# Kernel optimization log

Hardware: AMD Instinct MI355X
Metric: run time of the kernel (lower is better)

## Reference

```python
import jax, jax.numpy as jnp
import numpy as np

NUM_HEADS = 12
EPS = 1e-4


def setup_inputs() -> dict:
    key = jax.random.key(0)
    k1, k2, k3 = jax.random.split(key, 3)
    C = 768
    B, N = 128, 196  # B = b * num_frames = 8 * 16
    x = jax.random.normal(k1, (B, N, C), dtype=jnp.float32)
    W_qkv = jax.random.normal(k2, (3 * C, C), dtype=jnp.float32) * 0.02
    W_proj = jax.random.normal(k3, (C, C), dtype=jnp.float32) * 0.02
    b_proj = jnp.zeros((C,), dtype=jnp.float32)
    return {"x": x, "W_qkv": W_qkv, "W_proj": W_proj, "b_proj": b_proj,
            "num_frames": 16}


def reference(x, W_qkv, W_proj, b_proj, num_frames):
    B, N, C = x.shape
    h = NUM_HEADS
    e = C // h
    # qkv projection (no bias), split k-first then heads: 'b n (k h e)'
    qkv = (x @ W_qkv.T).reshape(B, N, 3, h, e)
    q, k, v = qkv[:, :, 0], qkv[:, :, 1], qkv[:, :, 2]  # [B, N, h, e]
    q_ = jax.nn.relu(q)
    k_ = jax.nn.relu(k)
    # fold frames into the sequence: (b f) n -> b (f n)
    b = B // num_frames
    S = num_frames * N
    q_ = q_.reshape(b, S, h, e)
    k_ = k_.reshape(b, S, h, e)
    v_ = v.reshape(b, S, h, e)
    # kv trick: kv[b,h,e,d] = sum_s k[b,s,h,e] v[b,s,h,d]
    kv = jnp.einsum('bshe,bshd->bhed', k_, v_)
    k_sum = k_.sum(axis=1)  # [b, h, e]
    z = 1.0 / (jnp.einsum('bshe,bhe->bsh', q_, k_sum) + EPS)  # [b, S, h]
    out = jnp.einsum('bshe,bhed->bshd', q_, kv) * z[..., None]  # [b, S, h, e]
    out = out.reshape(B, N, C)
    # output projection (dropouts are identity at eval)
    return out @ W_proj.T + b_proj
```

## Files before the change

### kernel.cpp

```cpp
#include <hip/hip_runtime.h>
#include <hip/hip_bf16.h>

#define EPS_Z 1e-4f

typedef __attribute__((ext_vector_type(8))) short bf16x8;
typedef __attribute__((ext_vector_type(4))) float f32x4;

__device__ __forceinline__ float b2f(short s) {
    union { unsigned u; float f; } cv;
    cv.u = ((unsigned)(unsigned short)s) << 16;
    return cv.f;
}

__device__ __forceinline__ void gld_lds16(const __hip_bfloat16* g, __hip_bfloat16* l) {
    __builtin_amdgcn_global_load_lds(
        (__attribute__((address_space(1))) void*)(g),
        (__attribute__((address_space(3))) void*)(l),
        16, 0, 0);
}

__global__ __launch_bounds__(256)
void cvt_f32_bf16(const float* __restrict__ in, __hip_bfloat16* __restrict__ out, int n4)
{
    int i = blockIdx.x * 256 + threadIdx.x;
    if (i >= n4) return;
    float4 v = ((const float4*)in)[i];
    union { short4 s; __hip_bfloat16 h[4]; } o;
    o.h[0] = __float2bfloat16(v.x);
    o.h[1] = __float2bfloat16(v.y);
    o.h[2] = __float2bfloat16(v.z);
    o.h[3] = __float2bfloat16(v.w);
    ((short4*)out)[i] = o.s;
}

template<int MODE, typename CT>
__global__ __launch_bounds__(256, 2)
void gemm_bt(const __hip_bfloat16* __restrict__ A,
             const __hip_bfloat16* __restrict__ B,
             CT* __restrict__ C,
             const float* __restrict__ bias,
             int K, int N, int gx)
{
    __shared__ __align__(16) __hip_bfloat16 As[128 * 64];
    __shared__ __align__(16) __hip_bfloat16 Bs[128 * 64];
    const int g = blockIdx.x;
    const int gp = (g & 7) * ((int)gridDim.x >> 3) + (g >> 3);
    const int bx = gp % gx;
    const int by = gp / gx;

    const int tid = threadIdx.x;
    const int w = tid >> 6;
    const int l = tid & 63;
    const int wr = (w >> 1) * 64;
    const int wc = (w & 1) * 64;
    const int l15 = l & 15;
    const int lq = l >> 4;
    const int rx = l15 & 7;

    f32x4 acc[4][4] = {};

    const int srow8 = l >> 3;
    const int scol = (((l & 7) ^ (l >> 3)) << 3);

    const __hip_bfloat16* Ab = A + (size_t)by * 128 * K;
    const __hip_bfloat16* Bb = B + (size_t)bx * 128 * K;

    for (int k0 = 0; k0 < K; k0 += 64) {
        __syncthreads();
        #pragma unroll
        for (int i = 0; i < 4; ++i) {
            const int chunk = w * 4 + i;
            const int row = chunk * 8 + srow8;
            gld_lds16(Ab + (size_t)row * K + (k0 + scol), As + chunk * 512);
            gld_lds16(Bb + (size_t)row * K + (k0 + scol), Bs + chunk * 512);
        }
        __syncthreads();
        #pragma unroll
        for (int kk = 0; kk < 64; kk += 32) {
            const int kb = (kk >> 3) + lq;
            const int col = (kb ^ rx) << 3;
            bf16x8 a[4], b[4];
            #pragma unroll
            for (int i = 0; i < 4; ++i)
                a[i] = *(const bf16x8*)(As + (wr + i * 16 + l15) * 64 + col);
            #pragma unroll
            for (int j = 0; j < 4; ++j)
                b[j] = *(const bf16x8*)(Bs + (wc + j * 16 + l15) * 64 + col);
            #pragma unroll
            for (int i = 0; i < 4; ++i)
                #pragma unroll
                for (int j = 0; j < 4; ++j)
                    acc[i][j] = __builtin_amdgcn_mfma_f32_16x16x32_bf16(a[i], b[j], acc[i][j], 0, 0, 0);
        }
    }

    const int crow0 = by * 128 + wr + lq * 4;
    const int ccol0 = bx * 128 + wc + l15;
    #pragma unroll
    for (int i = 0; i < 4; ++i) {
        #pragma unroll
        for (int j = 0; j < 4; ++j) {
            const int gc = ccol0 + j * 16;
            const float badd = (MODE == 2) ? bias[gc] : 0.0f;
            #pragma unroll
            for (int r = 0; r < 4; ++r) {
                const int gr = crow0 + i * 16 + r;
                float v = acc[i][j][r];
                if (MODE == 1 && gc < 1536) v = fmaxf(v, 0.0f);
                if (MODE == 2) v += badd;
                if (MODE == 1)
                    ((__hip_bfloat16*)C)[(size_t)gr * N + gc] = __float2bfloat16(v);
                else
                    ((float*)C)[(size_t)gr * N + gc] = v;
            }
        }
    }
}

__global__ __launch_bounds__(256)
void kv_mfma_kernel(const __hip_bfloat16* __restrict__ qkv,
                    float* __restrict__ kvg, float* __restrict__ ksumg)
{
    const int SPLIT = 14;
    const int bh = blockIdx.x / SPLIT;
    const int ck = blockIdx.x % SPLIT;
    const int b = bh / 12, h = bh % 12;

    __shared__ __align__(16) __hip_bfloat16 kT[64 * 40];
    __shared__ __align__(16) __hip_bfloat16 vT[64 * 40];

    const int tid = threadIdx.x;
    const int w = tid >> 6, l = tid & 63;
    const int l15 = l & 15, lq = l >> 4;

    const int half = tid >> 7;
    const int idx  = tid & 127;
    const int e0 = (idx >> 4) * 8;
    const int sp = idx & 15;

    const size_t rowbase = (size_t)b * 3136 * 2304 + (half ? 1536 : 768) + h * 64 + e0;
    __hip_bfloat16* Tdst = half ? vT : kT;

    f32x4 acc[4] = {};
    f32x4 accks = {};

    bf16x8 ones;
    #pragma unroll
    for (int i = 0; i < 8; ++i) ones[i] = (short)0x3F80;

    const int s_begin = ck * 224;
    for (int s0 = s_begin; s0 < s_begin + 224; s0 += 32) {
        __syncthreads();
        bf16x8 r0 = *(const bf16x8*)(qkv + rowbase + (size_t)(s0 + 2 * sp) * 2304);
        bf16x8 r1 = *(const bf16x8*)(qkv + rowbase + (size_t)(s0 + 2 * sp + 1) * 2304);
        #pragma unroll
        for (int q = 0; q < 8; ++q) {
            unsigned pk = ((unsigned)(unsigned short)r0[q]) |
                          (((unsigned)(unsigned short)r1[q]) << 16);
            *(unsigned*)(Tdst + (e0 + q) * 40 + 2 * sp) = pk;
        }
        __syncthreads();
        bf16x8 a = *(const bf16x8*)(vT + (w * 16 + l15) * 40 + lq * 8);
        bf16x8 bfr[4];
        #pragma unroll
        for (int j = 0; j < 4; ++j)
            bfr[j] = *(const bf16x8*)(kT + (j * 16 + l15) * 40 + lq * 8);
        #pragma unroll
        for (int j = 0; j < 4; ++j)
            acc[j] = __builtin_amdgcn_mfma_f32_16x16x32_bf16(a, bfr[j], acc[j], 0, 0, 0);
        accks = __builtin_amdgcn_mfma_f32_16x16x32_bf16(ones, bfr[w], accks, 0, 0, 0);
    }

    float* kvdst = kvg + ((size_t)bh << 12);
    #pragma unroll
    for (int j = 0; j < 4; ++j) {
        const int col = j * 16 + l15;
        #pragma unroll
        for (int r = 0; r < 4; ++r) {
            const int row = w * 16 + lq * 4 + r;
            atomicAdd(kvdst + row * 64 + col, acc[j][r]);
        }
    }
    if (lq == 0)
        atomicAdd(ksumg + (bh << 6) + w * 16 + l15, accks[0]);
}

__global__ __launch_bounds__(256)
void attn_mfma2(const __hip_bfloat16* __restrict__ qkv,
                const __hip_bfloat16* __restrict__ kvb,
                const float* __restrict__ ksumg,
                __hip_bfloat16* __restrict__ att)
{
    const int bh = blockIdx.x / 49;
    const int mt = blockIdx.x % 49;
    const int b = bh / 12, h = bh % 12;
    const int tid = threadIdx.x;
    const int w = tid >> 6, l = tid & 63;
    const int l15 = l & 15, lq = l >> 4;

    const size_t m0 = (size_t)b * 3136 + (size_t)mt * 64 + w * 16;

    const __hip_bfloat16* qrow = qkv + (m0 + l15) * 2304 + h * 64;
    bf16x8 aq0 = *(const bf16x8*)(qrow + lq * 8);
    bf16x8 aq1 = *(const bf16x8*)(qrow + 32 + lq * 8);

    const float* ks = ksumg + (bh << 6);
    float kse[8], kse1[8];
    *(float4*)(kse)      = *(const float4*)(ks + lq * 8);
    *(float4*)(kse + 4)  = *(const float4*)(ks + lq * 8 + 4);
    *(float4*)(kse1)     = *(const float4*)(ks + 32 + lq * 8);
    *(float4*)(kse1 + 4) = *(const float4*)(ks + 32 + lq * 8 + 4);
    float zp = 0.0f;
    #pragma unroll
    for (int j = 0; j < 8; ++j)
        zp += b2f(aq0[j]) * kse[j] + b2f(aq1[j]) * kse1[j];
    zp += __shfl_xor(zp, 16);
    zp += __shfl_xor(zp, 32);
    const float zr = 1.0f / (zp + EPS_Z);

    const __hip_bfloat16* kvh = kvb + ((size_t)bh << 12);
    f32x4 acc[4] = {};
    #pragma unroll
    for (int j = 0; j < 4; ++j) {
        bf16x8 b0 = *(const bf16x8*)(kvh + (j * 16 + l15) * 64 + lq * 8);
        bf16x8 b1 = *(const bf16x8*)(kvh + (j * 16 + l15) * 64 + 32 + lq * 8);
        acc[j] = __builtin_amdgcn_mfma_f32_16x16x32_bf16(aq0, b0, acc[j], 0, 0, 0);
        acc[j] = __builtin_amdgcn_mfma_f32_16x16x32_bf16(aq1, b1, acc[j], 0, 0, 0);
    }

    float zrow[4];
    #pragma unroll
    for (int r = 0; r < 4; ++r) zrow[r] = __shfl(zr, lq * 4 + r);

    #pragma unroll
    for (int j = 0; j < 4; ++j) {
        const int col = j * 16 + l15;
        #pragma unroll
        for (int r = 0; r < 4; ++r) {
            const int row = lq * 4 + r;
            att[(m0 + row) * 768 + h * 64 + col] = __float2bfloat16(acc[j][r] * zrow[r]);
        }
    }
}

extern "C" void kernel_launch(void* const* d_in, const int* in_sizes, int n_in,
                              void* d_out, int out_size, void* d_ws, size_t ws_size,
                              hipStream_t stream)
{
    const float* x      = (const float*)d_in[0];
    const float* W_qkv  = (const float*)d_in[1];
    const float* W_proj = (const float*)d_in[2];
    const float* b_proj = (const float*)d_in[3];
    float* out = (float*)d_out;

    const int M = 25088, K = 768, N1 = 2304, N2 = 768;

    __hip_bfloat16* qkv = (__hip_bfloat16*)d_ws;
    __hip_bfloat16* xb  = qkv + (size_t)M * N1;
    __hip_bfloat16* wqb = xb + (size_t)M * K;
    __hip_bfloat16* wpb = wqb + (size_t)N1 * K;
    float* kvg  = (float*)(wpb + (size_t)N2 * K);
    float* ksum = kvg + 96 * 4096;
    __hip_bfloat16* kvb = (__hip_bfloat16*)(ksum + 96 * 64);
    __hip_bfloat16* att = xb;

    hipMemsetAsync(kvg, 0, (size_t)(96 * 4096 + 96 * 64) * sizeof(float), stream);

    cvt_f32_bf16<<<(M * K / 4 + 255) / 256, 256, 0, stream>>>(x, xb, M * K / 4);
    cvt_f32_bf16<<<(N1 * K / 4 + 255) / 256, 256, 0, stream>>>(W_qkv, wqb, N1 * K / 4);
    cvt_f32_bf16<<<(N2 * K / 4 + 255) / 256, 256, 0, stream>>>(W_proj, wpb, N2 * K / 4);

    gemm_bt<1, __hip_bfloat16><<<(M / 128) * (N1 / 128), 256, 0, stream>>>(
        xb, wqb, qkv, nullptr, K, N1, N1 / 128);
    kv_mfma_kernel<<<96 * 14, 256, 0, stream>>>(qkv, kvg, ksum);
    cvt_f32_bf16<<<(96 * 4096 / 4 + 255) / 256, 256, 0, stream>>>(kvg, kvb, 96 * 4096 / 4);
    attn_mfma2<<<96 * 49, 256, 0, stream>>>(qkv, kvb, ksum, att);
    gemm_bt<2, float><<<(M / 128) * (N2 / 128), 256, 0, stream>>>(
        att, wpb, out, b_proj, K, N2, N2 / 128);
}
```

Baseline: 347.1 us.

## Replace QKV GEMM with 256x256 double-buffered pipelined MFMA kernel

Adds a new QKV projection GEMM that uses 256x256 tiles, 512 threads, double-buffered LDS filled by direct global-to-LDS loads, XOR-swizzled LDS layout, and interleaved staging with MFMA phases under explicit waitcnt, barriers and setprio. The ReLU on the q and k columns is applied in the epilogue. The aim is to raise MFMA utilization and overlap memory with compute for the largest GEMM. The cost is high LDS use (128KB per block) and heavy register pressure, and with 98*9 blocks the wave quantization across CUs may be uneven.

```diff
diff --git a/kernel.cpp b/kernel.cpp
--- a/kernel.cpp
+++ b/kernel.cpp
@@ -17,6 +17,14 @@
         (__attribute__((address_space(1))) void*)(g),
         (__attribute__((address_space(3))) void*)(l),
         16, 0, 0);
+}
+
+__device__ __forceinline__ void fence_barrier() {
+    asm volatile("" ::: "memory");
+    __builtin_amdgcn_sched_barrier(0);
+    __builtin_amdgcn_s_barrier();
+    __builtin_amdgcn_sched_barrier(0);
+    asm volatile("" ::: "memory");
 }
 
 __global__ __launch_bounds__(256)
@@ -31,6 +39,174 @@
     o.h[2] = __float2bfloat16(v.z);
     o.h[3] = __float2bfloat16(v.w);
     ((short4*)out)[i] = o.s;
+}
+
+__global__ __launch_bounds__(512, 2)
+void gemm256_relu(const __hip_bfloat16* __restrict__ A,
+                  const __hip_bfloat16* __restrict__ B,
+                  __hip_bfloat16* __restrict__ C,
+                  int K, int N, int gx)
+{
+    __shared__ __align__(16) __hip_bfloat16 As[2][256 * 64];
+    __shared__ __align__(16) __hip_bfloat16 Bs[2][256 * 64];
+
+    const int nwg = (int)gridDim.x;
+    const int g = blockIdx.x;
+    const int xcd = g & 7, lin = g >> 3;
+    const int q = nwg >> 3, r = nwg & 7;
+    const int gp = (xcd < r ? xcd * (q + 1) : r * (q + 1) + (xcd - r) * q) + lin;
+    const int bx = gp % gx, by = gp / gx;
+
+    const int tid = threadIdx.x;
+    const int w = tid >> 6, l = tid & 63;
+    const int l15 = l & 15, lq = l >> 4;
+    const int rx = l15 & 7;
+    const int wr = (w >> 2) * 128;
+    const int wc = (w & 3) * 64;
+    const int srow8 = l >> 3;
+    const int scol = ((l & 7) ^ srow8) << 3;
+
+    const __hip_bfloat16* Ab = A + (size_t)by * 256 * K;
+    const __hip_bfloat16* Bb = B + (size_t)bx * 256 * K;
+
+    f32x4 acc[8][4] = {};
+    const int NT = K >> 6;
+
+#define STAGE_A(buf_, half_, t_) do { \
+    const int k0_ = (t_) << 6; \
+    const int c0_ = (half_) * 16 + w * 2; \
+    gld_lds16(Ab + (size_t)(c0_ * 8 + srow8) * K + (k0_ + scol), &As[buf_][c0_ * 512]); \
+    gld_lds16(Ab + (size_t)((c0_ + 1) * 8 + srow8) * K + (k0_ + scol), &As[buf_][(c0_ + 1) * 512]); \
+} while (0)
+#define STAGE_B(buf_, half_, t_) do { \
+    const int k0_ = (t_) << 6; \
+    const int c0_ = (half_) * 16 + w * 2; \
+    gld_lds16(Bb + (size_t)(c0_ * 8 + srow8) * K + (k0_ + scol), &Bs[buf_][c0_ * 512]); \
+    gld_lds16(Bb + (size_t)((c0_ + 1) * 8 + srow8) * K + (k0_ + scol), &Bs[buf_][(c0_ + 1) * 512]); \
+} while (0)
+
+    STAGE_B(0, 0, 0); STAGE_B(0, 1, 0);
+    STAGE_A(0, 0, 0); STAGE_A(0, 1, 0);
+    STAGE_B(1, 0, 1); STAGE_B(1, 1, 1);
+    asm volatile("s_waitcnt vmcnt(4)" ::: "memory");
+    fence_barrier();
+
+    for (int t = 0; t < NT; ++t) {
+        const int buf = t & 1;
+        const __hip_bfloat16* Asb = As[buf];
+        const __hip_bfloat16* Bsb = Bs[buf];
+        bf16x8 bfr[4][2];
+        bf16x8 afr[2][2];
+
+        #pragma unroll
+        for (int j = 0; j < 4; ++j)
+            #pragma unroll
+            for (int ks = 0; ks < 2; ++ks)
+                bfr[j][ks] = *(const bf16x8*)(Bsb + (wc + j * 16 + l15) * 64 + (((ks * 4 + lq) ^ rx) << 3));
+        #pragma unroll
+        for (int d = 0; d < 2; ++d)
+            #pragma unroll
+            for (int ks = 0; ks < 2; ++ks)
+                afr[d][ks] = *(const bf16x8*)(Asb + (wr + (0 + d) * 16 + l15) * 64 + (((ks * 4 + lq) ^ rx) << 3));
+        if (t + 1 < NT) STAGE_A(buf ^ 1, 0, t + 1);
+        fence_barrier();
+        asm volatile("s_waitcnt lgkmcnt(0)" ::: "memory");
+        __builtin_amdgcn_sched_barrier(0);
+        __builtin_amdgcn_s_setprio(1);
+        #pragma unroll
+        for (int d = 0; d < 2; ++d)
+            #pragma unroll
+            for (int j = 0; j < 4; ++j)
+                #pragma unroll
+                for (int ks = 0; ks < 2; ++ks)
+                    acc[0 + d][j] = __builtin_amdgcn_mfma_f32_16x16x32_bf16(afr[d][ks], bfr[j][ks], acc[0 + d][j], 0, 0, 0);
+        __builtin_amdgcn_s_setprio(0);
+        fence_barrier();
+
+        #pragma unroll
+        for (int d = 0; d < 2; ++d)
+            #pragma unroll
+            for (int ks = 0; ks < 2; ++ks)
+                afr[d][ks] = *(const bf16x8*)(Asb + (wr + (2 + d) * 16 + l15) * 64 + (((ks * 4 + lq) ^ rx) << 3));
+        if (t + 1 < NT) STAGE_A(buf ^ 1, 1, t + 1);
+        fence_barrier();
+        asm volatile("s_waitcnt lgkmcnt(0)" ::: "memory");
+        __builtin_amdgcn_sched_barrier(0);
+        __builtin_amdgcn_s_setprio(1);
+        #pragma unroll
+        for (int d = 0; d < 2; ++d)
+            #pragma unroll
+            for (int j = 0; j < 4; ++j)
+                #pragma unroll
+                for (int ks = 0; ks < 2; ++ks)
+                    acc[2 + d][j] = __builtin_amdgcn_mfma_f32_16x16x32_bf16(afr[d][ks], bfr[j][ks], acc[2 + d][j], 0, 0, 0);
+        __builtin_amdgcn_s_setprio(0);
+        fence_barrier();
+
+        #pragma unroll
+        for (int d = 0; d < 2; ++d)
+            #pragma unroll
+            for (int ks = 0; ks < 2; ++ks)
+                afr[d][ks] = *(const bf16x8*)(Asb + (wr + (4 + d) * 16 + l15) * 64 + (((ks * 4 + lq) ^ rx) << 3));
+        if (t + 2 < NT) STAGE_B(buf, 0, t + 2);
+        fence_barrier();
+        asm volatile("s_waitcnt lgkmcnt(0)" ::: "memory");
+        __builtin_amdgcn_sched_barrier(0);
+        __builtin_amdgcn_s_setprio(1);
+        #pragma unroll
+        for (int d = 0; d < 2; ++d)
+            #pragma unroll
+            for (int j = 0; j < 4; ++j)
+                #pragma unroll
+                for (int ks = 0; ks < 2; ++ks)
+                    acc[4 + d][j] = __builtin_amdgcn_mfma_f32_16x16x32_bf16(afr[d][ks], bfr[j][ks], acc[4 + d][j], 0, 0, 0);
+        __builtin_amdgcn_s_setprio(0);
+        fence_barrier();
+
+        #pragma unroll
+        for (int d = 0; d < 2; ++d)
+            #pragma unroll
+            for (int ks = 0; ks < 2; ++ks)
+                afr[d][ks] = *(const bf16x8*)(Asb + (wr + (6 + d) * 16 + l15) * 64 + (((ks * 4 + lq) ^ rx) << 3));
+        if (t + 2 < NT) STAGE_B(buf, 1, t + 2);
+        fence_barrier();
+        asm volatile("s_waitcnt lgkmcnt(0)" ::: "memory");
+        __builtin_amdgcn_sched_barrier(0);
+        __builtin_amdgcn_s_setprio(1);
+        #pragma unroll
+        for (int d = 0; d < 2; ++d)
+            #pragma unroll
+            for (int j = 0; j < 4; ++j)
+                #pragma unroll
+                for (int ks = 0; ks < 2; ++ks)
+                    acc[6 + d][j] = __builtin_amdgcn_mfma_f32_16x16x32_bf16(afr[d][ks], bfr[j][ks], acc[6 + d][j], 0, 0, 0);
+        __builtin_amdgcn_s_setprio(0);
+        if (t < NT - 1) {
+            if (t == NT - 2) asm volatile("s_waitcnt vmcnt(0)" ::: "memory");
+            else             asm volatile("s_waitcnt vmcnt(4)" ::: "memory");
+            fence_barrier();
+        }
+    }
+
+#undef STAGE_A
+#undef STAGE_B
+
+    const int crow0 = by * 256 + wr + lq * 4;
+    const int ccol0 = bx * 256 + wc + l15;
+    #pragma unroll
+    for (int mi = 0; mi < 8; ++mi) {
+        #pragma unroll
+        for (int j = 0; j < 4; ++j) {
+            const int gc = ccol0 + j * 16;
+            #pragma unroll
+            for (int rr = 0; rr < 4; ++rr) {
+                const int gr = crow0 + mi * 16 + rr;
+                float v = acc[mi][j][rr];
+                if (gc < 1536) v = fmaxf(v, 0.0f);
+                C[(size_t)gr * N + gc] = __float2bfloat16(v);
+            }
+        }
+    }
 }
 
 template<int MODE, typename CT>
@@ -154,10 +330,10 @@
         bf16x8 r0 = *(const bf16x8*)(qkv + rowbase + (size_t)(s0 + 2 * sp) * 2304);
         bf16x8 r1 = *(const bf16x8*)(qkv + rowbase + (size_t)(s0 + 2 * sp + 1) * 2304);
         #pragma unroll
-        for (int q = 0; q < 8; ++q) {
-            unsigned pk = ((unsigned)(unsigned short)r0[q]) |
-                          (((unsigned)(unsigned short)r1[q]) << 16);
-            *(unsigned*)(Tdst + (e0 + q) * 40 + 2 * sp) = pk;
+        for (int qq = 0; qq < 8; ++qq) {
+            unsigned pk = ((unsigned)(unsigned short)r0[qq]) |
+                          (((unsigned)(unsigned short)r1[qq]) << 16);
+            *(unsigned*)(Tdst + (e0 + qq) * 40 + 2 * sp) = pk;
         }
         __syncthreads();
         bf16x8 a = *(const bf16x8*)(vT + (w * 16 + l15) * 40 + lq * 8);
@@ -270,8 +446,8 @@
     cvt_f32_bf16<<<(N1 * K / 4 + 255) / 256, 256, 0, stream>>>(W_qkv, wqb, N1 * K / 4);
     cvt_f32_bf16<<<(N2 * K / 4 + 255) / 256, 256, 0, stream>>>(W_proj, wpb, N2 * K / 4);
 
-    gemm_bt<1, __hip_bfloat16><<<(M / 128) * (N1 / 128), 256, 0, stream>>>(
-        xb, wqb, qkv, nullptr, K, N1, N1 / 128);
+    gemm256_relu<<<(M / 256) * (N1 / 256), 512, 0, stream>>>(
+        xb, wqb, qkv, K, N1, N1 / 256);
     kv_mfma_kernel<<<96 * 14, 256, 0, stream>>>(qkv, kvg, ksum);
     cvt_f32_bf16<<<(96 * 4096 / 4 + 255) / 256, 256, 0, stream>>>(kvg, kvb, 96 * 4096 / 4);
     attn_mfma2<<<96 * 49, 256, 0, stream>>>(qkv, kvb, ksum, att);
```

Result: slower. 370.6 us (+6.8%).
